# Kernel optimization log

Measured on AMD Instinct MI355X. Metric: run time of the kernel, lower is better.

Reference implementation:

```python
import jax, jax.numpy as jnp
import numpy as np

N = 50000      # num nodes
E = 800000     # num edges
F = 64         # in_channels
H = 4          # heads
C = 64         # out_channels
NEG_SLOPE = 0.2
SCALE = float(np.sqrt(F))  # scaled_product=True -> divide by sqrt(in_channels)


def setup_inputs() -> dict:
    key = jax.random.key(0)
    k1, k2, k3, k4, k5, k6 = jax.random.split(key, 6)
    x = jax.random.normal(k1, (N, F), dtype=jnp.float32)
    edge_index = jax.random.randint(k2, (2, E), 0, N, dtype=jnp.int32)
    edge_weight = jax.random.uniform(k3, (E, 1), dtype=jnp.float32)
    # learned parameters (glorot-ish scale)
    W_lin = jax.random.normal(k4, (F, H * C), dtype=jnp.float32) / np.sqrt(F)
    W_att = jax.random.normal(k5, (F, H * F), dtype=jnp.float32) / np.sqrt(F)
    bias = jnp.zeros((H * C,), dtype=jnp.float32)
    return {"x": x, "edge_index": edge_index, "edge_weight": edge_weight,
            "W_lin": W_lin, "W_att": W_att, "bias": bias}


def reference(x, edge_index, edge_weight, W_lin, W_att, bias):
    src = edge_index[0]  # j: source / message sender
    dst = edge_index[1]  # i: target / aggregation index

    # node transforms
    xs = (x @ W_lin).reshape(N, H, C)   # lin(x): values for messages
    u = (x @ W_att).reshape(N, H, F)    # lin_att(x): multiplicative attention keys

    # multiplicative attention score: x_j^T W_h x_i  -> [E, H]
    score = jnp.einsum('ehf,ef->eh', u[src], x[dst]) / SCALE
    score = jax.nn.leaky_relu(score, NEG_SLOPE)

    # masked scatter-softmax over incoming edges of each destination node
    smax = jax.ops.segment_max(jax.lax.stop_gradient(score), dst, num_segments=N)  # [N, H]
    e = jnp.exp(score - smax[dst]) * edge_weight                                   # mask = edge_weight
    denom = jax.ops.segment_sum(e, dst, num_segments=N) + 1e-16                    # [N, H]
    alpha = e / denom[dst]                                                         # [E, H]

    # message = alpha * x_src, aggregate (add) at destination
    out = jax.ops.segment_sum(alpha[:, :, None] * xs[src], dst, num_segments=N)    # [N, H, C]
    out = out.reshape(N, H * C) + bias                                             # concat heads + bias
    return out
```

## Files before the change

### kernel.cpp

```cpp
#include <hip/hip_runtime.h>
#include <hip/hip_bf16.h>
#include <math.h>

#define N_NODES 50000
#define N_EDGES 800000
#define GEMM_ROWS 32
#define AGG_NODES 32
#define PAD_EDGES (N_EDGES + N_NODES * 15)
#define SCALE_FOLD 0.18033688011112042f
#define XT_STRIDE 68

typedef __attribute__((ext_vector_type(8))) short bf16x8_t;
typedef __attribute__((ext_vector_type(4))) float f32x4_t;

static __device__ __forceinline__ ushort bfrn(float v) {
  __hip_bfloat16 b = __float2bfloat16(v);
  return __builtin_bit_cast(ushort, b);
}
static __device__ __forceinline__ uint packbf(float v) {
  ushort h = bfrn(v);
  float r = v - __uint_as_float((uint)h << 16);
  return (uint)h | ((uint)bfrn(r) << 16);
}
static __device__ __forceinline__ bf16x8_t as_bf16x8(uint4 u) {
  union { uint4 a; bf16x8_t b; } c; c.a = u; return c.b;
}
static __device__ __forceinline__ bf16x8_t as_bf16x8w(uint w0, uint w1,
                                                     uint w2, uint w3) {
  union { uint4 a; bf16x8_t b; } c; c.a = make_uint4(w0, w1, w2, w3); return c.b;
}
static __device__ __forceinline__ float bflo(uint u) {
  return __uint_as_float(u << 16);
}
static __device__ __forceinline__ float bfhi(uint u) {
  return __uint_as_float(u & 0xFFFF0000u);
}

__global__ __launch_bounds__(256) void hist_kernel(
    const int* __restrict__ dst, int* __restrict__ deg, int* __restrict__ epos,
    const float* __restrict__ Watt, float* __restrict__ Wt) {
  int e = blockIdx.x * 256 + threadIdx.x;
  if (e < 16384) {
    int h = e & 3;
    int g = (e >> 2) & 63;
    int f = e >> 8;
    Wt[e] = Watt[g * 256 + h * 64 + f] * SCALE_FOLD;
  }
  if (e < N_EDGES) epos[e] = atomicAdd(&deg[dst[e]], 1);
}

__global__ __launch_bounds__(256) void base_kernel(
    const int* __restrict__ deg, int* __restrict__ cursor,
    int2* __restrict__ offs2, int2* __restrict__ csr2) {
  const int i = blockIdx.x * 256 + threadIdx.x;
  const int lane = threadIdx.x & 63;
  const int d = (i < N_NODES) ? deg[i] : 0;
  const int nt = (d + 15) >> 4;
  const int pd = nt << 4;
  int incl = pd;
#pragma unroll
  for (int m = 1; m < 64; m <<= 1) {
    int u = __shfl_up(incl, m);
    if (lane >= m) incl += u;
  }
  int wbase = 0;
  if (lane == 63) wbase = atomicAdd(cursor, incl);
  wbase = __shfl(wbase, 63);
  const int base = wbase + incl - pd;
  if (i < N_NODES) {
    offs2[i] = make_int2(base, nt);
    for (int j = d; j < pd; ++j) csr2[base + j] = make_int2(0, 0);
  }
}

__global__ __launch_bounds__(256) void scatter_kernel(
    const int* __restrict__ src, const int* __restrict__ dst,
    const float* __restrict__ ew, const int2* __restrict__ offs2,
    const int* __restrict__ epos, int2* __restrict__ csr2) {
  int e = blockIdx.x * 256 + threadIdx.x;
  if (e >= N_EDGES) return;
  int idx = offs2[dst[e]].x + epos[e];
  csr2[idx] = make_int2(src[e], __float_as_int(ew[e]));
}

__global__ __launch_bounds__(256) void qgemm_kernel(
    const float* __restrict__ x, const float* __restrict__ Wt,
    uint4* __restrict__ q_packed, ushort* __restrict__ xhi) {
  __shared__ float xlds[GEMM_ROWS * 64];
  const int tid = threadIdx.x;
  const int blk = blockIdx.x;
#pragma unroll
  for (int p = 0; p < 8; ++p) {
    int idx = p * 256 + tid;
    int gidx = blk * (GEMM_ROWS * 64) + idx;
    xlds[idx] = (gidx < N_NODES * 64) ? x[gidx] : 0.f;
  }
  __syncthreads();
  {
    int row = tid >> 3;
    int c0 = (tid & 7) * 8;
    int grow = blk * GEMM_ROWS + row;
    if (grow < N_NODES) {
      uint hu[4];
#pragma unroll
      for (int d2 = 0; d2 < 4; ++d2) {
        float v0 = xlds[row * 64 + c0 + 2 * d2];
        float v1 = xlds[row * 64 + c0 + 2 * d2 + 1];
        hu[d2] = (uint)bfrn(v0) | ((uint)bfrn(v1) << 16);
      }
      *(uint4*)(xhi + (size_t)grow * 64 + c0) =
          make_uint4(hu[0], hu[1], hu[2], hu[3]);
    }
  }
  const int c4 = tid & 63;
  const int rg = (tid >> 6) * 8;
  const float4* Wv = (const float4*)Wt;
  float4 acc[8] = {};
  for (int k = 0; k < 64; ++k) {
    float4 w4 = Wv[(size_t)k * 64 + c4];
#pragma unroll
    for (int r = 0; r < 8; ++r) {
      float a = xlds[(rg + r) * 64 + k];
      acc[r].x += a * w4.x; acc[r].y += a * w4.y;
      acc[r].z += a * w4.z; acc[r].w += a * w4.w;
    }
  }
#pragma unroll
  for (int r = 0; r < 8; ++r) {
    int row = blk * GEMM_ROWS + rg + r;
    if (row < N_NODES) {
      uint4 pk;
      pk.x = packbf(acc[r].x); pk.y = packbf(acc[r].y);
      pk.z = packbf(acc[r].z); pk.w = packbf(acc[r].w);
      q_packed[(size_t)row * 64 + c4] = pk;
    }
  }
}

__global__ __launch_bounds__(256) void aggregate_kernel(
    const uint4* __restrict__ qp4, const uint4* __restrict__ xhi4,
    const int2* __restrict__ offs2, const int2* __restrict__ csr2,
    ushort* __restrict__ agg) {
  __shared__ uint qlds[4][256];
  __shared__ __attribute__((aligned(16))) float xt[4][16][XT_STRIDE];
  __shared__ __attribute__((aligned(16))) float plds[4][16][4];
  const int wave = threadIdx.x >> 6;
  const int node = blockIdx.x * 4 + wave;
  const int lane = threadIdx.x & 63;
  const int l15 = lane & 15;
  const int lg = lane >> 4;
  const int hq = l15 & 3;

  *(uint4*)&qlds[wave][lane * 4] = qp4[(size_t)node * 64 + lane];
  const int2 o2 = offs2[node];

  uint qh0[4], ql0[4], qh1[4], ql1[4];
#pragma unroll
  for (int d = 0; d < 4; ++d) {
    uint a0 = qlds[wave][(8 * lg + 2 * d) * 4 + hq];
    uint b0 = qlds[wave][(8 * lg + 2 * d + 1) * 4 + hq];
    qh0[d] = (a0 & 0xFFFFu) | (b0 << 16);
    ql0[d] = (a0 >> 16) | (b0 & 0xFFFF0000u);
    uint a1 = qlds[wave][(32 + 8 * lg + 2 * d) * 4 + hq];
    uint b1 = qlds[wave][(32 + 8 * lg + 2 * d + 1) * 4 + hq];
    qh1[d] = (a1 & 0xFFFFu) | (b1 << 16);
    ql1[d] = (a1 >> 16) | (b1 & 0xFFFF0000u);
  }
  const bf16x8_t Qh0 = as_bf16x8w(qh0[0], qh0[1], qh0[2], qh0[3]);
  const bf16x8_t Qh1 = as_bf16x8w(qh1[0], qh1[1], qh1[2], qh1[3]);
  const bf16x8_t Ql0 = as_bf16x8w(ql0[0], ql0[1], ql0[2], ql0[3]);
  const bf16x8_t Ql1 = as_bf16x8w(ql1[0], ql1[1], ql1[2], ql1[3]);

  const int s0 = o2.x;
  const int ntiles = o2.y;

  f32x4_t acc = {0.f, 0.f, 0.f, 0.f};
  float Lp = 0.f;

  for (int t = 0; t < ntiles; ++t) {
    const int k0 = s0 + t * 16;
    const int2 e2 = csr2[k0 + l15];
    const int j = e2.x;
    const float w = __int_as_float(e2.y);
    const uint4 ah0 = xhi4[(size_t)j * 8 + lg];
    const uint4 ah1 = xhi4[(size_t)j * 8 + 4 + lg];
    f32x4_t S = {0.f, 0.f, 0.f, 0.f};
    S = __builtin_amdgcn_mfma_f32_16x16x32_bf16(Qh0, as_bf16x8(ah0), S, 0, 0, 0);
    S = __builtin_amdgcn_mfma_f32_16x16x32_bf16(Qh1, as_bf16x8(ah1), S, 0, 0, 0);
    S = __builtin_amdgcn_mfma_f32_16x16x32_bf16(Ql0, as_bf16x8(ah0), S, 0, 0, 0);
    S = __builtin_amdgcn_mfma_f32_16x16x32_bf16(Ql1, as_bf16x8(ah1), S, 0, 0, 0);
    float xf[16];
    xf[0] = bflo(ah0.x);  xf[1] = bfhi(ah0.x);
    xf[2] = bflo(ah0.y);  xf[3] = bfhi(ah0.y);
    xf[4] = bflo(ah0.z);  xf[5] = bfhi(ah0.z);
    xf[6] = bflo(ah0.w);  xf[7] = bfhi(ah0.w);
    xf[8] = bflo(ah1.x);  xf[9] = bfhi(ah1.x);
    xf[10] = bflo(ah1.y); xf[11] = bfhi(ah1.y);
    xf[12] = bflo(ah1.z); xf[13] = bfhi(ah1.z);
    xf[14] = bflo(ah1.w); xf[15] = bfhi(ah1.w);
    *(float4*)&xt[wave][l15][8 * lg + 0] =
        make_float4(xf[0], xf[1], xf[2], xf[3]);
    *(float4*)&xt[wave][l15][8 * lg + 4] =
        make_float4(xf[4], xf[5], xf[6], xf[7]);
    *(float4*)&xt[wave][l15][32 + 8 * lg + 0] =
        make_float4(xf[8], xf[9], xf[10], xf[11]);
    *(float4*)&xt[wave][l15][32 + 8 * lg + 4] =
        make_float4(xf[12], xf[13], xf[14], xf[15]);
    float p0 = exp2f(fmaxf(S[0], 0.2f * S[0])) * w;
    float p1 = exp2f(fmaxf(S[1], 0.2f * S[1])) * w;
    float p2 = exp2f(fmaxf(S[2], 0.2f * S[2])) * w;
    float p3 = exp2f(fmaxf(S[3], 0.2f * S[3])) * w;
    if (lg == 0) *(float4*)&plds[wave][l15][0] = make_float4(p0, p1, p2, p3);
#pragma unroll
    for (int e = 0; e < 16; ++e) {
      float4 xv = *(const float4*)&xt[wave][e][l15 * 4];
      float pe = plds[wave][e][lg];
      acc[0] += pe * xv.x; acc[1] += pe * xv.y;
      acc[2] += pe * xv.z; acc[3] += pe * xv.w;
      Lp += pe;
    }
  }

  const float inv = 1.f / (Lp + 1e-16f);
  uint w0 = (uint)bfrn(acc[0] * inv) | ((uint)bfrn(acc[1] * inv) << 16);
  uint w1 = (uint)bfrn(acc[2] * inv) | ((uint)bfrn(acc[3] * inv) << 16);
  *(uint2*)(agg + (size_t)node * 256 + lg * 64 + l15 * 4) = make_uint2(w0, w1);
}

__global__ __launch_bounds__(256) void out_gemm_kernel(
    const ushort* __restrict__ agg, const float* __restrict__ Wlin,
    const float* __restrict__ bias, float* __restrict__ out) {
  __shared__ float4 atile[AGG_NODES][4][17];
  const int tid = threadIdx.x;
  const int node0 = blockIdx.x * AGG_NODES;
  const uint2* av = (const uint2*)agg;
#pragma unroll
  for (int p = 0; p < 8; ++p) {
    int idx = p * 256 + tid;
    int row = idx >> 6;
    int cc = idx & 63;
    if (node0 + row < N_NODES) {
      uint2 u = av[(size_t)(node0 + row) * 64 + cc];
      float4 f;
      f.x = bflo(u.x); f.y = bfhi(u.x);
      f.z = bflo(u.y); f.w = bfhi(u.y);
      atile[row][cc >> 4][cc & 15] = f;
    }
  }
  __syncthreads();
  const int c4 = tid & 63;
  const int ns = tid >> 6;
  const int hh = c4 >> 4;
  const float4* Wv = (const float4*)Wlin;
  float4 acc[8] = {};
  for (int g4 = 0; g4 < 16; ++g4) {
    float4 w0 = Wv[(size_t)(g4 * 4 + 0) * 64 + c4];
    float4 w1 = Wv[(size_t)(g4 * 4 + 1) * 64 + c4];
    float4 w2 = Wv[(size_t)(g4 * 4 + 2) * 64 + c4];
    float4 w3 = Wv[(size_t)(g4 * 4 + 3) * 64 + c4];
#pragma unroll
    for (int n = 0; n < 8; ++n) {
      float4 a = atile[ns * 8 + n][hh][g4];
      acc[n].x += a.x * w0.x + a.y * w1.x + a.z * w2.x + a.w * w3.x;
      acc[n].y += a.x * w0.y + a.y * w1.y + a.z * w2.y + a.w * w3.y;
      acc[n].z += a.x * w0.z + a.y * w1.z + a.z * w2.z + a.w * w3.z;
      acc[n].w += a.x * w0.w + a.y * w1.w + a.z * w2.w + a.w * w3.w;
    }
  }
  float4 bv = ((const float4*)bias)[c4];
#pragma unroll
  for (int n = 0; n < 8; ++n) {
    int node = node0 + ns * 8 + n;
    if (node < N_NODES) {
      float4 o;
      o.x = acc[n].x + bv.x; o.y = acc[n].y + bv.y;
      o.z = acc[n].z + bv.z; o.w = acc[n].w + bv.w;
      ((float4*)out)[(size_t)node * 64 + c4] = o;
    }
  }
}

extern "C" void kernel_launch(void* const* d_in, const int* in_sizes, int n_in,
                              void* d_out, int out_size, void* d_ws,
                              size_t ws_size, hipStream_t stream) {
  (void)in_sizes; (void)n_in; (void)out_size; (void)ws_size;
  const float* x    = (const float*)d_in[0];
  const int*   ei   = (const int*)d_in[1];
  const float* ew   = (const float*)d_in[2];
  const float* Wlin = (const float*)d_in[3];
  const float* Watt = (const float*)d_in[4];
  const float* bias = (const float*)d_in[5];
  float* out = (float*)d_out;

  const int* srcv = ei;
  const int* dstv = ei + N_EDGES;

  char* ws = (char*)d_ws;
  size_t off = 0;
  auto alloc = [&](size_t bytes) {
    void* p = ws + off;
    off += (bytes + 255) & ~(size_t)255;
    return p;
  };
  uint*   q_packed = (uint*)alloc((size_t)N_NODES * 256 * 4);
  ushort* agg      = (ushort*)alloc((size_t)N_NODES * 256 * 2);
  ushort* xhi      = (ushort*)alloc((size_t)N_NODES * 64 * 2);
  int2*   offs2    = (int2*)alloc((size_t)N_NODES * 8);
  int2*   csr2     = (int2*)alloc((size_t)PAD_EDGES * 8);
  char* aggc = (char*)agg;
  int*   deg    = (int*)aggc;
  int*   cursor = (int*)(aggc + N_NODES * 4);
  int*   epos   = (int*)(aggc + 256 * 1024);
  float* Wt     = (float*)(aggc + 4 * 1024 * 1024);

  hipMemsetAsync(deg, 0, (size_t)(N_NODES + 64) * 4, stream);

  hist_kernel<<<(N_EDGES + 255) / 256, 256, 0, stream>>>(dstv, deg, epos,
                                                         Watt, Wt);
  base_kernel<<<(N_NODES + 255) / 256, 256, 0, stream>>>(deg, cursor, offs2,
                                                         csr2);
  scatter_kernel<<<(N_EDGES + 255) / 256, 256, 0, stream>>>(
      srcv, dstv, ew, offs2, epos, csr2);
  qgemm_kernel<<<(N_NODES + GEMM_ROWS - 1) / GEMM_ROWS, 256, 0, stream>>>(
      x, Wt, (uint4*)q_packed, xhi);
  aggregate_kernel<<<N_NODES / 4, 256, 0, stream>>>(
      (const uint4*)q_packed, (const uint4*)xhi, offs2, csr2, agg);
  out_gemm_kernel<<<(N_NODES + AGG_NODES - 1) / AGG_NODES, 256, 0, stream>>>(
      agg, Wlin, bias, out);
}
```

Baseline: 176.0 us.

## Drop split-bf16 query, pre-transpose Q layout, merge qgemm with CSR base kernel

The query projection is now stored as plain bf16 instead of a hi/lo bf16 pair. That halves Q storage and cuts the score MFMAs per tile from four to two. The attention weight matrix is pre-transposed so each lane can load its MFMA A-operand directly from global memory, removing the LDS staging and repacking. The LDS x tile keeps packed bf16 and unpacks it at use, and the qgemm and CSR base-offset kernels are merged into one launch. The cost is lower score precision, which may affect accuracy.

```diff
diff --git a/kernel.cpp b/kernel.cpp
--- a/kernel.cpp
+++ b/kernel.cpp
@@ -7,8 +7,10 @@
 #define GEMM_ROWS 32
 #define AGG_NODES 32
 #define PAD_EDGES (N_EDGES + N_NODES * 15)
+#define QGEMM_BLOCKS ((N_NODES + GEMM_ROWS - 1) / GEMM_ROWS)
+#define BASE_BLOCKS ((N_NODES + 255) / 256)
 #define SCALE_FOLD 0.18033688011112042f
-#define XT_STRIDE 68
+#define XT_STRIDE 36
 
 typedef __attribute__((ext_vector_type(8))) short bf16x8_t;
 typedef __attribute__((ext_vector_type(4))) float f32x4_t;
@@ -17,17 +19,8 @@
   __hip_bfloat16 b = __float2bfloat16(v);
   return __builtin_bit_cast(ushort, b);
 }
-static __device__ __forceinline__ uint packbf(float v) {
-  ushort h = bfrn(v);
-  float r = v - __uint_as_float((uint)h << 16);
-  return (uint)h | ((uint)bfrn(r) << 16);
-}
 static __device__ __forceinline__ bf16x8_t as_bf16x8(uint4 u) {
   union { uint4 a; bf16x8_t b; } c; c.a = u; return c.b;
-}
-static __device__ __forceinline__ bf16x8_t as_bf16x8w(uint w0, uint w1,
-                                                     uint w2, uint w3) {
-  union { uint4 a; bf16x8_t b; } c; c.a = make_uint4(w0, w1, w2, w3); return c.b;
 }
 static __device__ __forceinline__ float bflo(uint u) {
   return __uint_as_float(u << 16);
@@ -41,35 +34,91 @@
     const float* __restrict__ Watt, float* __restrict__ Wt) {
   int e = blockIdx.x * 256 + threadIdx.x;
   if (e < 16384) {
-    int h = e & 3;
-    int g = (e >> 2) & 63;
-    int f = e >> 8;
-    Wt[e] = Watt[g * 256 + h * 64 + f] * SCALE_FOLD;
+    int c = e & 63;
+    int r = (e >> 6) & 63;
+    int h = e >> 12;
+    Wt[e] = Watt[c * 256 + h * 64 + r] * SCALE_FOLD;
   }
   if (e < N_EDGES) epos[e] = atomicAdd(&deg[dst[e]], 1);
 }
 
-__global__ __launch_bounds__(256) void base_kernel(
+__global__ __launch_bounds__(256) void qgemm_base_kernel(
+    const float* __restrict__ x, const float* __restrict__ Wt,
+    uint2* __restrict__ q_t2, ushort* __restrict__ xhi,
     const int* __restrict__ deg, int* __restrict__ cursor,
     int2* __restrict__ offs2, int2* __restrict__ csr2) {
-  const int i = blockIdx.x * 256 + threadIdx.x;
-  const int lane = threadIdx.x & 63;
-  const int d = (i < N_NODES) ? deg[i] : 0;
-  const int nt = (d + 15) >> 4;
-  const int pd = nt << 4;
-  int incl = pd;
-#pragma unroll
-  for (int m = 1; m < 64; m <<= 1) {
-    int u = __shfl_up(incl, m);
-    if (lane >= m) incl += u;
-  }
-  int wbase = 0;
-  if (lane == 63) wbase = atomicAdd(cursor, incl);
-  wbase = __shfl(wbase, 63);
-  const int base = wbase + incl - pd;
-  if (i < N_NODES) {
-    offs2[i] = make_int2(base, nt);
-    for (int j = d; j < pd; ++j) csr2[base + j] = make_int2(0, 0);
+  const int tid = threadIdx.x;
+  if (blockIdx.x >= QGEMM_BLOCKS) {
+    const int i = (blockIdx.x - QGEMM_BLOCKS) * 256 + tid;
+    const int lane = tid & 63;
+    const int d = (i < N_NODES) ? deg[i] : 0;
+    const int nt = (d + 15) >> 4;
+    const int pd = nt << 4;
+    int incl = pd;
+#pragma unroll
+    for (int m = 1; m < 64; m <<= 1) {
+      int u = __shfl_up(incl, m);
+      if (lane >= m) incl += u;
+    }
+    int wbase = 0;
+    if (lane == 63) wbase = atomicAdd(cursor, incl);
+    wbase = __shfl(wbase, 63);
+    const int base = wbase + incl - pd;
+    if (i < N_NODES) {
+      offs2[i] = make_int2(base, nt);
+      for (int j = d; j < pd; ++j) csr2[base + j] = make_int2(0, 0);
+    }
+    return;
+  }
+  __shared__ float xlds[GEMM_ROWS * 64];
+  const int blk = blockIdx.x;
+#pragma unroll
+  for (int p = 0; p < 8; ++p) {
+    int idx = p * 256 + tid;
+    int gidx = blk * (GEMM_ROWS * 64) + idx;
+    xlds[idx] = (gidx < N_NODES * 64) ? x[gidx] : 0.f;
+  }
+  __syncthreads();
+  {
+    int row = tid >> 3;
+    int c0 = (tid & 7) * 8;
+    int grow = blk * GEMM_ROWS + row;
+    if (grow < N_NODES) {
+      uint hu[4];
+#pragma unroll
+      for (int d2 = 0; d2 < 4; ++d2) {
+        float v0 = xlds[row * 64 + c0 + 2 * d2];
+        float v1 = xlds[row * 64 + c0 + 2 * d2 + 1];
+        hu[d2] = (uint)bfrn(v0) | ((uint)bfrn(v1) << 16);
+      }
+      *(uint4*)(xhi + (size_t)grow * 64 + c0) =
+          make_uint4(hu[0], hu[1], hu[2], hu[3]);
+    }
+  }
+  const int c4 = tid & 63;
+  const int h = c4 >> 4;
+  const int f4 = c4 & 15;
+  const int rg = (tid >> 6) * 8;
+  const float4* Wv = (const float4*)Wt;
+  float4 acc[8] = {};
+  for (int g = 0; g < 64; ++g) {
+    float4 w4 = Wv[(size_t)h * 1024 + g * 16 + f4];
+#pragma unroll
+    for (int r = 0; r < 8; ++r) {
+      float a = xlds[(rg + r) * 64 + g];
+      acc[r].x += a * w4.x; acc[r].y += a * w4.y;
+      acc[r].z += a * w4.z; acc[r].w += a * w4.w;
+    }
+  }
+#pragma unroll
+  for (int r = 0; r < 8; ++r) {
+    int row = blk * GEMM_ROWS + rg + r;
+    if (row < N_NODES) {
+      uint2 pk;
+      pk.x = (uint)bfrn(acc[r].x) | ((uint)bfrn(acc[r].y) << 16);
+      pk.y = (uint)bfrn(acc[r].z) | ((uint)bfrn(acc[r].w) << 16);
+      q_t2[(size_t)row * 64 + c4] = pk;
+    }
   }
 }
 
@@ -83,66 +132,11 @@
   csr2[idx] = make_int2(src[e], __float_as_int(ew[e]));
 }
 
-__global__ __launch_bounds__(256) void qgemm_kernel(
-    const float* __restrict__ x, const float* __restrict__ Wt,
-    uint4* __restrict__ q_packed, ushort* __restrict__ xhi) {
-  __shared__ float xlds[GEMM_ROWS * 64];
-  const int tid = threadIdx.x;
-  const int blk = blockIdx.x;
-#pragma unroll
-  for (int p = 0; p < 8; ++p) {
-    int idx = p * 256 + tid;
-    int gidx = blk * (GEMM_ROWS * 64) + idx;
-    xlds[idx] = (gidx < N_NODES * 64) ? x[gidx] : 0.f;
-  }
-  __syncthreads();
-  {
-    int row = tid >> 3;
-    int c0 = (tid & 7) * 8;
-    int grow = blk * GEMM_ROWS + row;
-    if (grow < N_NODES) {
-      uint hu[4];
-#pragma unroll
-      for (int d2 = 0; d2 < 4; ++d2) {
-        float v0 = xlds[row * 64 + c0 + 2 * d2];
-        float v1 = xlds[row * 64 + c0 + 2 * d2 + 1];
-        hu[d2] = (uint)bfrn(v0) | ((uint)bfrn(v1) << 16);
-      }
-      *(uint4*)(xhi + (size_t)grow * 64 + c0) =
-          make_uint4(hu[0], hu[1], hu[2], hu[3]);
-    }
-  }
-  const int c4 = tid & 63;
-  const int rg = (tid >> 6) * 8;
-  const float4* Wv = (const float4*)Wt;
-  float4 acc[8] = {};
-  for (int k = 0; k < 64; ++k) {
-    float4 w4 = Wv[(size_t)k * 64 + c4];
-#pragma unroll
-    for (int r = 0; r < 8; ++r) {
-      float a = xlds[(rg + r) * 64 + k];
-      acc[r].x += a * w4.x; acc[r].y += a * w4.y;
-      acc[r].z += a * w4.z; acc[r].w += a * w4.w;
-    }
-  }
-#pragma unroll
-  for (int r = 0; r < 8; ++r) {
-    int row = blk * GEMM_ROWS + rg + r;
-    if (row < N_NODES) {
-      uint4 pk;
-      pk.x = packbf(acc[r].x); pk.y = packbf(acc[r].y);
-      pk.z = packbf(acc[r].z); pk.w = packbf(acc[r].w);
-      q_packed[(size_t)row * 64 + c4] = pk;
-    }
-  }
-}
-
 __global__ __launch_bounds__(256) void aggregate_kernel(
-    const uint4* __restrict__ qp4, const uint4* __restrict__ xhi4,
+    const uint4* __restrict__ qt4, const uint4* __restrict__ xhi4,
     const int2* __restrict__ offs2, const int2* __restrict__ csr2,
     ushort* __restrict__ agg) {
-  __shared__ uint qlds[4][256];
-  __shared__ __attribute__((aligned(16))) float xt[4][16][XT_STRIDE];
+  __shared__ __attribute__((aligned(16))) uint xt[4][16][XT_STRIDE];
   __shared__ __attribute__((aligned(16))) float plds[4][16][4];
   const int wave = threadIdx.x >> 6;
   const int node = blockIdx.x * 4 + wave;
@@ -151,26 +145,11 @@
   const int lg = lane >> 4;
   const int hq = l15 & 3;
 
-  *(uint4*)&qlds[wave][lane * 4] = qp4[(size_t)node * 64 + lane];
+  const bf16x8_t Qa =
+      as_bf16x8(qt4[(size_t)node * 32 + hq * 8 + lg]);
+  const bf16x8_t Qb =
+      as_bf16x8(qt4[(size_t)node * 32 + hq * 8 + 4 + lg]);
   const int2 o2 = offs2[node];
-
-  uint qh0[4], ql0[4], qh1[4], ql1[4];
-#pragma unroll
-  for (int d = 0; d < 4; ++d) {
-    uint a0 = qlds[wave][(8 * lg + 2 * d) * 4 + hq];
-    uint b0 = qlds[wave][(8 * lg + 2 * d + 1) * 4 + hq];
-    qh0[d] = (a0 & 0xFFFFu) | (b0 << 16);
-    ql0[d] = (a0 >> 16) | (b0 & 0xFFFF0000u);
-    uint a1 = qlds[wave][(32 + 8 * lg + 2 * d) * 4 + hq];
-    uint b1 = qlds[wave][(32 + 8 * lg + 2 * d + 1) * 4 + hq];
-    qh1[d] = (a1 & 0xFFFFu) | (b1 << 16);
-    ql1[d] = (a1 >> 16) | (b1 & 0xFFFF0000u);
-  }
-  const bf16x8_t Qh0 = as_bf16x8w(qh0[0], qh0[1], qh0[2], qh0[3]);
-  const bf16x8_t Qh1 = as_bf16x8w(qh1[0], qh1[1], qh1[2], qh1[3]);
-  const bf16x8_t Ql0 = as_bf16x8w(ql0[0], ql0[1], ql0[2], ql0[3]);
-  const bf16x8_t Ql1 = as_bf16x8w(ql1[0], ql1[1], ql1[2], ql1[3]);
-
   const int s0 = o2.x;
   const int ntiles = o2.y;
 
@@ -184,28 +163,11 @@
     const float w = __int_as_float(e2.y);
     const uint4 ah0 = xhi4[(size_t)j * 8 + lg];
     const uint4 ah1 = xhi4[(size_t)j * 8 + 4 + lg];
+    *(uint4*)&xt[wave][l15][4 * lg] = ah0;
+    *(uint4*)&xt[wave][l15][16 + 4 * lg] = ah1;
     f32x4_t S = {0.f, 0.f, 0.f, 0.f};
-    S = __builtin_amdgcn_mfma_f32_16x16x32_bf16(Qh0, as_bf16x8(ah0), S, 0, 0, 0);
-    S = __builtin_amdgcn_mfma_f32_16x16x32_bf16(Qh1, as_bf16x8(ah1), S, 0, 0, 0);
-    S = __builtin_amdgcn_mfma_f32_16x16x32_bf16(Ql0, as_bf16x8(ah0), S, 0, 0, 0);
-    S = __builtin_amdgcn_mfma_f32_16x16x32_bf16(Ql1, as_bf16x8(ah1), S, 0, 0, 0);
-    float xf[16];
-    xf[0] = bflo(ah0.x);  xf[1] = bfhi(ah0.x);
-    xf[2] = bflo(ah0.y);  xf[3] = bfhi(ah0.y);
-    xf[4] = bflo(ah0.z);  xf[5] = bfhi(ah0.z);
-    xf[6] = bflo(ah0.w);  xf[7] = bfhi(ah0.w);
-    xf[8] = bflo(ah1.x);  xf[9] = bfhi(ah1.x);
-    xf[10] = bflo(ah1.y); xf[11] = bfhi(ah1.y);
-    xf[12] = bflo(ah1.z); xf[13] = bfhi(ah1.z);
-    xf[14] = bflo(ah1.w); xf[15] = bfhi(ah1.w);
-    *(float4*)&xt[wave][l15][8 * lg + 0] =
-        make_float4(xf[0], xf[1], xf[2], xf[3]);
-    *(float4*)&xt[wave][l15][8 * lg + 4] =
-        make_float4(xf[4], xf[5], xf[6], xf[7]);
-    *(float4*)&xt[wave][l15][32 + 8 * lg + 0] =
-        make_float4(xf[8], xf[9], xf[10], xf[11]);
-    *(float4*)&xt[wave][l15][32 + 8 * lg + 4] =
-        make_float4(xf[12], xf[13], xf[14], xf[15]);
+    S = __builtin_amdgcn_mfma_f32_16x16x32_bf16(Qa, as_bf16x8(ah0), S, 0, 0, 0);
+    S = __builtin_amdgcn_mfma_f32_16x16x32_bf16(Qb, as_bf16x8(ah1), S, 0, 0, 0);
     float p0 = exp2f(fmaxf(S[0], 0.2f * S[0])) * w;
     float p1 = exp2f(fmaxf(S[1], 0.2f * S[1])) * w;
     float p2 = exp2f(fmaxf(S[2], 0.2f * S[2])) * w;
@@ -213,10 +175,12 @@
     if (lg == 0) *(float4*)&plds[wave][l15][0] = make_float4(p0, p1, p2, p3);
 #pragma unroll
     for (int e = 0; e < 16; ++e) {
-      float4 xv = *(const float4*)&xt[wave][e][l15 * 4];
+      uint2 xw = *(const uint2*)&xt[wave][e][2 * l15];
       float pe = plds[wave][e][lg];
-      acc[0] += pe * xv.x; acc[1] += pe * xv.y;
-      acc[2] += pe * xv.z; acc[3] += pe * xv.w;
+      acc[0] += pe * bflo(xw.x);
+      acc[1] += pe * bfhi(xw.x);
+      acc[2] += pe * bflo(xw.y);
+      acc[3] += pe * bfhi(xw.y);
       Lp += pe;
     }
   }
@@ -302,11 +266,11 @@
     off += (bytes + 255) & ~(size_t)255;
     return p;
   };
-  uint*   q_packed = (uint*)alloc((size_t)N_NODES * 256 * 4);
-  ushort* agg      = (ushort*)alloc((size_t)N_NODES * 256 * 2);
-  ushort* xhi      = (ushort*)alloc((size_t)N_NODES * 64 * 2);
-  int2*   offs2    = (int2*)alloc((size_t)N_NODES * 8);
-  int2*   csr2     = (int2*)alloc((size_t)PAD_EDGES * 8);
+  ushort* q_t   = (ushort*)alloc((size_t)N_NODES * 256 * 2);
+  ushort* agg   = (ushort*)alloc((size_t)N_NODES * 256 * 2);
+  ushort* xhi   = (ushort*)alloc((size_t)N_NODES * 64 * 2);
+  int2*   offs2 = (int2*)alloc((size_t)N_NODES * 8);
+  int2*   csr2  = (int2*)alloc((size_t)PAD_EDGES * 8);
   char* aggc = (char*)agg;
   int*   deg    = (int*)aggc;
   int*   cursor = (int*)(aggc + N_NODES * 4);
@@ -317,14 +281,12 @@
 
   hist_kernel<<<(N_EDGES + 255) / 256, 256, 0, stream>>>(dstv, deg, epos,
                                                          Watt, Wt);
-  base_kernel<<<(N_NODES + 255) / 256, 256, 0, stream>>>(deg, cursor, offs2,
-                                                         csr2);
+  qgemm_base_kernel<<<QGEMM_BLOCKS + BASE_BLOCKS, 256, 0, stream>>>(
+      x, Wt, (uint2*)q_t, xhi, deg, cursor, offs2, csr2);
   scatter_kernel<<<(N_EDGES + 255) / 256, 256, 0, stream>>>(
       srcv, dstv, ew, offs2, epos, csr2);
-  qgemm_kernel<<<(N_NODES + GEMM_ROWS - 1) / GEMM_ROWS, 256, 0, stream>>>(
-      x, Wt, (uint4*)q_packed, xhi);
   aggregate_kernel<<<N_NODES / 4, 256, 0, stream>>>(
-      (const uint4*)q_packed, (const uint4*)xhi, offs2, csr2, agg);
+      (const uint4*)q_t, (const uint4*)xhi, offs2, csr2, agg);
   out_gemm_kernel<<<(N_NODES + AGG_NODES - 1) / AGG_NODES, 256, 0, stream>>>(
       agg, Wlin, bias, out);
 }
```

Result: faster. 170.9 us (-2.9%).
